# Kernel tuning notes

Hardware: AMD Instinct MI355X
Metric: run time of the kernel (lower is better)

Reference implementation:

```python
import jax, jax.numpy as jnp
import numpy as np

WALL_COT = 0.5   # init kwarg wall_cot
N_SEG = 64       # number of distinct segment ids (matches fill_max of segs)
MIN_FRAC = 0.01  # thresholds used in the torch loop


def _nearest_ds(x, He, We):
    """F.interpolate(x, size=(He,We), mode='nearest').squeeze(1) for x:[B,1,H,W].
    torch nearest picks src index floor(dst * H/He)."""
    B, _, H, W = x.shape
    iy = (jnp.arange(He) * H) // He
    ix = (jnp.arange(We) * W) // We
    return x[:, 0][:, iy][:, :, ix]  # [B,He,We]


def setup_inputs() -> dict:
    key = jax.random.key(0)
    ks = jax.random.split(key, 6)
    B, C_img, H, W = 8, 3, 512, 512
    C_feat, He, We = 64, 128, 128
    return {
        "outputs": jax.random.normal(ks[0], (B, C_img, H, W), dtype=jnp.float32),
        "inputs": jax.random.normal(ks[1], (B, C_img, H, W), dtype=jnp.float32),
        "enc1": jax.random.normal(ks[2], (B, C_feat, He, We), dtype=jnp.float32),
        "dec1": jax.random.normal(ks[3], (B, C_feat, He, We), dtype=jnp.float32),
        "masks": jax.random.uniform(ks[4], (B, 1, H, W), dtype=jnp.float32),
        "segs": jax.random.randint(ks[5], (B, 1, H, W), 0, N_SEG, dtype=jnp.int32),
        "confidence": jnp.zeros((1,), dtype=jnp.float32),
        "iteration": 1,
        "epoch": 0,
    }


def reference(outputs, inputs, enc1, dec1, masks, segs, confidence, iteration, epoch):
    B, _, He, We = enc1.shape
    npix = He * We

    # nearest-neighbor downsample of segment ids and cost masks to feature res
    seg_i = _nearest_ds(segs, He, We)            # [B,He,We] int
    mask_i = _nearest_ds(masks, He, We)          # [B,He,We]

    # per-pixel reconstruction error, mean over channels
    reco_error = jnp.mean((enc1 - dec1) ** 2, axis=1)  # [B,He,We]

    # segmented reductions: offset segment ids per batch item -> one flat pass
    flat_seg = (jnp.arange(B, dtype=jnp.int32)[:, None] * N_SEG
                + seg_i.reshape(B, -1)).reshape(-1)       # [B*He*We]
    f32 = reco_error.dtype
    counts = jax.ops.segment_sum(jnp.ones_like(flat_seg, dtype=f32), flat_seg,
                                 num_segments=B * N_SEG)  # [B*N_SEG]
    sum_err = jax.ops.segment_sum(reco_error.reshape(-1), flat_seg,
                                  num_segments=B * N_SEG)
    pos_px = ((mask_i > 0) & (mask_i < WALL_COT)).reshape(-1).astype(f32)
    pos_cnt = jax.ops.segment_sum(pos_px, flat_seg, num_segments=B * N_SEG)

    safe_cnt = jnp.maximum(counts, 1.0)
    mean_err = sum_err / safe_cnt                  # mean reco error per segment
    valid = (counts / npix) >= MIN_FRAC            # torch: skip if count frac < 0.01
    pos_flag = (pos_cnt / safe_cnt) > MIN_FRAC     # torch: pos/counts > 0.01
    sel = (valid & pos_flag).astype(f32)
    # flat_reco_error_pos.mean()
    flat_pos_mean = jnp.sum(mean_err * sel) / jnp.maximum(jnp.sum(sel), 1.0)

    # recovery loss: zero-out targets where mask >= wall_cot, masked mean
    targets = jnp.where(masks >= WALL_COT, jnp.zeros_like(inputs), inputs)  # bcast [B,1,H,W]
    mse_recov = jnp.sum((outputs - targets) ** 2, axis=1, keepdims=True)    # [B,1,H,W]
    m = (masks > 0).astype(f32)
    loss_recov = jnp.sum(mse_recov * m) / jnp.maximum(jnp.sum(m), 1.0)

    return loss_recov + flat_pos_mean
```

## Files before the change

kernel.cpp:

```cpp
#include <hip/hip_runtime.h>

#define BATCH   8
#define CIMG    3
#define HFULL   512
#define WFULL   512
#define HWFULL  (HFULL * WFULL)
#define CFEAT   64
#define HE      128
#define WE      128
#define HWE     (HE * WE)
#define NSEG    64
#define NBSEG   (BATCH * NSEG)
#define WALL_COT 0.5f
#define MIN_FRAC 0.01f

#define NBLK    2048

#define WS_CNT   0
#define WS_SUM   NBSEG
#define WS_POS   (2 * NBSEG)
#define WS_BNUM  (3 * NBSEG)
#define WS_BDEN  (3 * NBSEG + NBLK)
#define WS_ZERO_FLOATS (3 * NBSEG)

__global__ __launch_bounds__(256, 2) void confloss_main_kernel(
    const float* __restrict__ outputs, const float* __restrict__ inputs,
    const float* __restrict__ enc1,    const float* __restrict__ dec1,
    const float* __restrict__ masks,   const int* __restrict__ segs,
    float* __restrict__ ws)
{
    const int tid = threadIdx.x;
    const int i   = blockIdx.x * 256 + tid;

    __shared__ float s_cnt[NSEG], s_sum[NSEG], s_pos[NSEG];
    __shared__ float s_rn[4], s_rd[4];
    if (tid < NSEG) { s_cnt[tid] = 0.f; s_sum[tid] = 0.f; s_pos[tid] = 0.f; }
    __syncthreads();

    const int g  = i & 32767;
    const int c  = i >> 15;
    const int ba = g >> 12;
    const int ra = (g & 4095) * 4;
    const size_t abase = ((size_t)ba * CFEAT + (size_t)c * 4) * HWE + ra;
    const float* ep = enc1 + abase;
    const float* dp = dec1 + abase;
    const int ya = ra >> 7, xa = ra & (WE - 1);
    const int fb = ba * HWFULL + (ya * 4) * WFULL + xa * 4;
    const bool duty = (c == (g & 15));

    const int bb = i >> 16;
    const int rb = (i & 65535) * 4;
    const float* ob = outputs + (size_t)bb * (CIMG * HWFULL) + rb;
    const float* ib = inputs  + (size_t)bb * (CIMG * HWFULL) + rb;

    const float4 e0 = *(const float4*)(ep);
    const float4 e1 = *(const float4*)(ep + HWE);
    const float4 e2 = *(const float4*)(ep + 2 * HWE);
    const float4 e3 = *(const float4*)(ep + 3 * HWE);
    const float4 d0 = *(const float4*)(dp);
    const float4 d1 = *(const float4*)(dp + HWE);
    const float4 d2 = *(const float4*)(dp + 2 * HWE);
    const float4 d3 = *(const float4*)(dp + 3 * HWE);
    const float4 mB = *(const float4*)(masks + (size_t)bb * HWFULL + rb);
    const float4 o0 = *(const float4*)(ob);
    const float4 o1 = *(const float4*)(ob + HWFULL);
    const float4 o2 = *(const float4*)(ob + 2 * HWFULL);
    const float4 i0 = *(const float4*)(ib);
    const float4 i1 = *(const float4*)(ib + HWFULL);
    const float4 i2 = *(const float4*)(ib + 2 * HWFULL);
    const int s0 = segs[fb], s1 = segs[fb + 4], s2 = segs[fb + 8], s3 = segs[fb + 12];
    float mk0 = 1.f, mk1 = 1.f, mk2 = 1.f, mk3 = 1.f;
    if (duty) {
        mk0 = masks[fb];     mk1 = masks[fb + 4];
        mk2 = masks[fb + 8]; mk3 = masks[fb + 12];
    }

    float num = 0.f, den = 0.f;
    {
        float tgt, dd, mse;
        mse = 0.f;
        tgt = (mB.x >= WALL_COT) ? 0.f : i0.x; dd = o0.x - tgt; mse += dd * dd;
        tgt = (mB.x >= WALL_COT) ? 0.f : i1.x; dd = o1.x - tgt; mse += dd * dd;
        tgt = (mB.x >= WALL_COT) ? 0.f : i2.x; dd = o2.x - tgt; mse += dd * dd;
        if (mB.x > 0.f) { num += mse; den += 1.f; }
        mse = 0.f;
        tgt = (mB.y >= WALL_COT) ? 0.f : i0.y; dd = o0.y - tgt; mse += dd * dd;
        tgt = (mB.y >= WALL_COT) ? 0.f : i1.y; dd = o1.y - tgt; mse += dd * dd;
        tgt = (mB.y >= WALL_COT) ? 0.f : i2.y; dd = o2.y - tgt; mse += dd * dd;
        if (mB.y > 0.f) { num += mse; den += 1.f; }
        mse = 0.f;
        tgt = (mB.z >= WALL_COT) ? 0.f : i0.z; dd = o0.z - tgt; mse += dd * dd;
        tgt = (mB.z >= WALL_COT) ? 0.f : i1.z; dd = o1.z - tgt; mse += dd * dd;
        tgt = (mB.z >= WALL_COT) ? 0.f : i2.z; dd = o2.z - tgt; mse += dd * dd;
        if (mB.z > 0.f) { num += mse; den += 1.f; }
        mse = 0.f;
        tgt = (mB.w >= WALL_COT) ? 0.f : i0.w; dd = o0.w - tgt; mse += dd * dd;
        tgt = (mB.w >= WALL_COT) ? 0.f : i1.w; dd = o1.w - tgt; mse += dd * dd;
        tgt = (mB.w >= WALL_COT) ? 0.f : i2.w; dd = o2.w - tgt; mse += dd * dd;
        if (mB.w > 0.f) { num += mse; den += 1.f; }
    }

    {
        float t0, t1, t2, t3;
        t0 = e0.x - d0.x; t1 = e1.x - d1.x; t2 = e2.x - d2.x; t3 = e3.x - d3.x;
        const float p0 = (t0*t0 + t1*t1 + t2*t2 + t3*t3) * (1.0f / (float)CFEAT);
        t0 = e0.y - d0.y; t1 = e1.y - d1.y; t2 = e2.y - d2.y; t3 = e3.y - d3.y;
        const float p1 = (t0*t0 + t1*t1 + t2*t2 + t3*t3) * (1.0f / (float)CFEAT);
        t0 = e0.z - d0.z; t1 = e1.z - d1.z; t2 = e2.z - d2.z; t3 = e3.z - d3.z;
        const float p2 = (t0*t0 + t1*t1 + t2*t2 + t3*t3) * (1.0f / (float)CFEAT);
        t0 = e0.w - d0.w; t1 = e1.w - d1.w; t2 = e2.w - d2.w; t3 = e3.w - d3.w;
        const float p3 = (t0*t0 + t1*t1 + t2*t2 + t3*t3) * (1.0f / (float)CFEAT);
        atomicAdd(&s_sum[s0], p0);
        atomicAdd(&s_sum[s1], p1);
        atomicAdd(&s_sum[s2], p2);
        atomicAdd(&s_sum[s3], p3);
        if (duty) {
            atomicAdd(&s_cnt[s0], 1.f); if (mk0 > 0.f && mk0 < WALL_COT) atomicAdd(&s_pos[s0], 1.f);
            atomicAdd(&s_cnt[s1], 1.f); if (mk1 > 0.f && mk1 < WALL_COT) atomicAdd(&s_pos[s1], 1.f);
            atomicAdd(&s_cnt[s2], 1.f); if (mk2 > 0.f && mk2 < WALL_COT) atomicAdd(&s_pos[s2], 1.f);
            atomicAdd(&s_cnt[s3], 1.f); if (mk3 > 0.f && mk3 < WALL_COT) atomicAdd(&s_pos[s3], 1.f);
        }
    }

#pragma unroll
    for (int off = 32; off >= 1; off >>= 1) {
        num += __shfl_down(num, off);
        den += __shfl_down(den, off);
    }
    if ((tid & 63) == 0) { s_rn[tid >> 6] = num; s_rd[tid >> 6] = den; }
    __syncthreads();

    if (tid == 0) {
        ws[WS_BNUM + blockIdx.x] = s_rn[0] + s_rn[1] + s_rn[2] + s_rn[3];
        ws[WS_BDEN + blockIdx.x] = s_rd[0] + s_rd[1] + s_rd[2] + s_rd[3];
    }
    if (tid < NSEG) {
        const int gb = ba * NSEG + tid;
        atomicAdd(&ws[WS_SUM + gb], s_sum[tid]);
        const float cv = s_cnt[tid];
        if (cv != 0.f) atomicAdd(&ws[WS_CNT + gb], cv);
        const float pv = s_pos[tid];
        if (pv != 0.f) atomicAdd(&ws[WS_POS + gb], pv);
    }
}

__global__ __launch_bounds__(512) void confloss_finalize_kernel(
    const float* __restrict__ ws, float* __restrict__ out)
{
    const int t = threadIdx.x;
    float rn = 0.f, rd = 0.f;
#pragma unroll
    for (int k = 0; k < NBLK / 512; ++k) {
        rn += ws[WS_BNUM + t + k * 512];
        rd += ws[WS_BDEN + t + k * 512];
    }
    const float cnt = ws[WS_CNT + t];
    const float sum = ws[WS_SUM + t];
    const float pos = ws[WS_POS + t];
    const float safe = fmaxf(cnt, 1.0f);
    const float mean = sum / safe;
    const bool valid = (cnt / (float)HWE) >= MIN_FRAC;
    const bool posf  = (pos / safe) > MIN_FRAC;
    float sel = (valid && posf) ? 1.0f : 0.0f;
    float val = mean * sel;

#pragma unroll
    for (int off = 32; off >= 1; off >>= 1) {
        val += __shfl_down(val, off);
        sel += __shfl_down(sel, off);
        rn  += __shfl_down(rn,  off);
        rd  += __shfl_down(rd,  off);
    }
    __shared__ float sv[8], ss[8], sn[8], sd[8];
    const int wid = t >> 6;
    if ((t & 63) == 0) { sv[wid] = val; ss[wid] = sel; sn[wid] = rn; sd[wid] = rd; }
    __syncthreads();
    if (t == 0) {
        float tv = 0.f, ts = 0.f, tn = 0.f, td = 0.f;
#pragma unroll
        for (int w = 0; w < 8; ++w) { tv += sv[w]; ts += ss[w]; tn += sn[w]; td += sd[w]; }
        const float flat_pos_mean = tv / fmaxf(ts, 1.0f);
        const float loss_recov = tn / fmaxf(td, 1.0f);
        out[0] = loss_recov + flat_pos_mean;
    }
}

extern "C" void kernel_launch(void* const* d_in, const int* in_sizes, int n_in,
                              void* d_out, int out_size, void* d_ws, size_t ws_size,
                              hipStream_t stream) {
    const float* outputs = (const float*)d_in[0];
    const float* inputs  = (const float*)d_in[1];
    const float* enc1    = (const float*)d_in[2];
    const float* dec1    = (const float*)d_in[3];
    const float* masks   = (const float*)d_in[4];
    const int*   segs    = (const int*)d_in[5];
    float* ws  = (float*)d_ws;
    float* out = (float*)d_out;

    hipMemsetAsync(ws, 0, WS_ZERO_FLOATS * sizeof(float), stream);

    confloss_main_kernel<<<NBLK, 256, 0, stream>>>(
        outputs, inputs, enc1, dec1, masks, segs, ws);
    confloss_finalize_kernel<<<1, 512, 0, stream>>>(ws, out);
}
```

Measured before the change: 36.68 us.

## Stream enc/dec tiles via global_load_lds, per-wave shared bins, replicated global bins

Enc1/dec1 feature loads now go straight into LDS through the async global_load_lds builtin, which frees VGPRs. The other loads are pinned with empty asm and a single vmcnt wait so they all stay in flight together. Per-segment error sums in shared memory are split per wave to cut LDS atomic contention. Global segment bins are replicated 8 ways by block index to spread the global atomic traffic, and finalize sums the replicas. This costs 32KB of extra LDS per block, which may lower occupancy, and it relies on a hand-placed waitcnt.

```diff
diff --git a/kernel.cpp b/kernel.cpp
--- a/kernel.cpp
+++ b/kernel.cpp
@@ -1,4 +1,5 @@
 #include <hip/hip_runtime.h>
+#include <stdint.h>
 
 #define BATCH   8
 #define CIMG    3
@@ -15,13 +16,17 @@
 #define MIN_FRAC 0.01f
 
 #define NBLK    2048
-
-#define WS_CNT   0
-#define WS_SUM   NBSEG
-#define WS_POS   (2 * NBSEG)
-#define WS_BNUM  (3 * NBSEG)
-#define WS_BDEN  (3 * NBSEG + NBLK)
-#define WS_ZERO_FLOATS (3 * NBSEG)
+#define NREP    8
+
+#define WS_BINS_FLOATS (NREP * 3 * NBSEG)
+#define WS_BNUM  WS_BINS_FLOATS
+#define WS_BDEN  (WS_BINS_FLOATS + NBLK)
+#define WS_ZERO_FLOATS WS_BINS_FLOATS
+
+#define KEEPF4(v) asm volatile("" :: "v"((v).x), "v"((v).y), "v"((v).z), "v"((v).w))
+
+typedef uint32_t u32g __attribute__((address_space(1)));
+typedef uint32_t u32l __attribute__((address_space(3)));
 
 __global__ __launch_bounds__(256, 2) void confloss_main_kernel(
     const float* __restrict__ outputs, const float* __restrict__ inputs,
@@ -30,11 +35,17 @@
     float* __restrict__ ws)
 {
     const int tid = threadIdx.x;
+    const int w   = tid >> 6;
+    const int l   = tid & 63;
     const int i   = blockIdx.x * 256 + tid;
 
-    __shared__ float s_cnt[NSEG], s_sum[NSEG], s_pos[NSEG];
+    __shared__ float sA[4][8][256];
+    __shared__ float s_sumW[4][NSEG];
+    __shared__ float s_cnt[NSEG], s_pos[NSEG];
     __shared__ float s_rn[4], s_rd[4];
-    if (tid < NSEG) { s_cnt[tid] = 0.f; s_sum[tid] = 0.f; s_pos[tid] = 0.f; }
+
+    s_sumW[w][l] = 0.f;
+    if (tid < NSEG) { s_cnt[tid] = 0.f; s_pos[tid] = 0.f; }
     __syncthreads();
 
     const int g  = i & 32767;
@@ -44,23 +55,28 @@
     const size_t abase = ((size_t)ba * CFEAT + (size_t)c * 4) * HWE + ra;
     const float* ep = enc1 + abase;
     const float* dp = dec1 + abase;
-    const int ya = ra >> 7, xa = ra & (WE - 1);
-    const int fb = ba * HWFULL + (ya * 4) * WFULL + xa * 4;
-    const bool duty = (c == (g & 15));
+
+#if __has_builtin(__builtin_amdgcn_global_load_lds)
+#pragma unroll
+    for (int k = 0; k < 4; ++k)
+        __builtin_amdgcn_global_load_lds((const u32g*)(ep + (size_t)k * HWE),
+                                         (u32l*)(&sA[w][k][0]), 16, 0, 0);
+#pragma unroll
+    for (int k = 0; k < 4; ++k)
+        __builtin_amdgcn_global_load_lds((const u32g*)(dp + (size_t)k * HWE),
+                                         (u32l*)(&sA[w][4 + k][0]), 16, 0, 0);
+#else
+#pragma unroll
+    for (int k = 0; k < 4; ++k) {
+        *(float4*)&sA[w][k][l * 4]     = *(const float4*)(ep + (size_t)k * HWE);
+        *(float4*)&sA[w][4 + k][l * 4] = *(const float4*)(dp + (size_t)k * HWE);
+    }
+#endif
 
     const int bb = i >> 16;
     const int rb = (i & 65535) * 4;
     const float* ob = outputs + (size_t)bb * (CIMG * HWFULL) + rb;
     const float* ib = inputs  + (size_t)bb * (CIMG * HWFULL) + rb;
-
-    const float4 e0 = *(const float4*)(ep);
-    const float4 e1 = *(const float4*)(ep + HWE);
-    const float4 e2 = *(const float4*)(ep + 2 * HWE);
-    const float4 e3 = *(const float4*)(ep + 3 * HWE);
-    const float4 d0 = *(const float4*)(dp);
-    const float4 d1 = *(const float4*)(dp + HWE);
-    const float4 d2 = *(const float4*)(dp + 2 * HWE);
-    const float4 d3 = *(const float4*)(dp + 3 * HWE);
     const float4 mB = *(const float4*)(masks + (size_t)bb * HWFULL + rb);
     const float4 o0 = *(const float4*)(ob);
     const float4 o1 = *(const float4*)(ob + HWFULL);
@@ -68,13 +84,22 @@
     const float4 i0 = *(const float4*)(ib);
     const float4 i1 = *(const float4*)(ib + HWFULL);
     const float4 i2 = *(const float4*)(ib + 2 * HWFULL);
+
+    const int ya = ra >> 7, xa = ra & (WE - 1);
+    const int fb = ba * HWFULL + (ya * 4) * WFULL + xa * 4;
     const int s0 = segs[fb], s1 = segs[fb + 4], s2 = segs[fb + 8], s3 = segs[fb + 12];
+    const bool duty = (c == (g & 15));
     float mk0 = 1.f, mk1 = 1.f, mk2 = 1.f, mk3 = 1.f;
     if (duty) {
         mk0 = masks[fb];     mk1 = masks[fb + 4];
         mk2 = masks[fb + 8]; mk3 = masks[fb + 12];
     }
 
+    KEEPF4(mB); KEEPF4(o0); KEEPF4(o1); KEEPF4(o2);
+    KEEPF4(i0); KEEPF4(i1); KEEPF4(i2);
+    asm volatile("" :: "v"(s0), "v"(s1), "v"(s2), "v"(s3));
+    asm volatile("s_waitcnt vmcnt(0)" ::: "memory");
+
     float num = 0.f, den = 0.f;
     {
         float tgt, dd, mse;
@@ -101,19 +126,29 @@
     }
 
     {
+        const float4 E0 = *(const float4*)&sA[w][0][l * 4];
+        const float4 E1 = *(const float4*)&sA[w][1][l * 4];
+        const float4 E2 = *(const float4*)&sA[w][2][l * 4];
+        const float4 E3 = *(const float4*)&sA[w][3][l * 4];
+        const float4 D0 = *(const float4*)&sA[w][4][l * 4];
+        const float4 D1 = *(const float4*)&sA[w][5][l * 4];
+        const float4 D2 = *(const float4*)&sA[w][6][l * 4];
+        const float4 D3 = *(const float4*)&sA[w][7][l * 4];
+
         float t0, t1, t2, t3;
-        t0 = e0.x - d0.x; t1 = e1.x - d1.x; t2 = e2.x - d2.x; t3 = e3.x - d3.x;
+        t0 = E0.x - D0.x; t1 = E1.x - D1.x; t2 = E2.x - D2.x; t3 = E3.x - D3.x;
         const float p0 = (t0*t0 + t1*t1 + t2*t2 + t3*t3) * (1.0f / (float)CFEAT);
-        t0 = e0.y - d0.y; t1 = e1.y - d1.y; t2 = e2.y - d2.y; t3 = e3.y - d3.y;
+        t0 = E0.y - D0.y; t1 = E1.y - D1.y; t2 = E2.y - D2.y; t3 = E3.y - D3.y;
         const float p1 = (t0*t0 + t1*t1 + t2*t2 + t3*t3) * (1.0f / (float)CFEAT);
-        t0 = e0.z - d0.z; t1 = e1.z - d1.z; t2 = e2.z - d2.z; t3 = e3.z - d3.z;
+        t0 = E0.z - D0.z; t1 = E1.z - D1.z; t2 = E2.z - D2.z; t3 = E3.z - D3.z;
         const float p2 = (t0*t0 + t1*t1 + t2*t2 + t3*t3) * (1.0f / (float)CFEAT);
-        t0 = e0.w - d0.w; t1 = e1.w - d1.w; t2 = e2.w - d2.w; t3 = e3.w - d3.w;
+        t0 = E0.w - D0.w; t1 = E1.w - D1.w; t2 = E2.w - D2.w; t3 = E3.w - D3.w;
         const float p3 = (t0*t0 + t1*t1 + t2*t2 + t3*t3) * (1.0f / (float)CFEAT);
-        atomicAdd(&s_sum[s0], p0);
-        atomicAdd(&s_sum[s1], p1);
-        atomicAdd(&s_sum[s2], p2);
-        atomicAdd(&s_sum[s3], p3);
+
+        atomicAdd(&s_sumW[w][s0], p0);
+        atomicAdd(&s_sumW[w][s1], p1);
+        atomicAdd(&s_sumW[w][s2], p2);
+        atomicAdd(&s_sumW[w][s3], p3);
         if (duty) {
             atomicAdd(&s_cnt[s0], 1.f); if (mk0 > 0.f && mk0 < WALL_COT) atomicAdd(&s_pos[s0], 1.f);
             atomicAdd(&s_cnt[s1], 1.f); if (mk1 > 0.f && mk1 < WALL_COT) atomicAdd(&s_pos[s1], 1.f);
@@ -127,7 +162,7 @@
         num += __shfl_down(num, off);
         den += __shfl_down(den, off);
     }
-    if ((tid & 63) == 0) { s_rn[tid >> 6] = num; s_rd[tid >> 6] = den; }
+    if (l == 0) { s_rn[w] = num; s_rd[w] = den; }
     __syncthreads();
 
     if (tid == 0) {
@@ -135,12 +170,15 @@
         ws[WS_BDEN + blockIdx.x] = s_rd[0] + s_rd[1] + s_rd[2] + s_rd[3];
     }
     if (tid < NSEG) {
+        const int rep  = blockIdx.x & (NREP - 1);
+        float* bins = ws + rep * (3 * NBSEG);
         const int gb = ba * NSEG + tid;
-        atomicAdd(&ws[WS_SUM + gb], s_sum[tid]);
+        const float sv = s_sumW[0][tid] + s_sumW[1][tid] + s_sumW[2][tid] + s_sumW[3][tid];
+        if (sv != 0.f) atomicAdd(&bins[NBSEG + gb], sv);
         const float cv = s_cnt[tid];
-        if (cv != 0.f) atomicAdd(&ws[WS_CNT + gb], cv);
+        if (cv != 0.f) atomicAdd(&bins[gb], cv);
         const float pv = s_pos[tid];
-        if (pv != 0.f) atomicAdd(&ws[WS_POS + gb], pv);
+        if (pv != 0.f) atomicAdd(&bins[2 * NBSEG + gb], pv);
     }
 }
 
@@ -154,9 +192,14 @@
         rn += ws[WS_BNUM + t + k * 512];
         rd += ws[WS_BDEN + t + k * 512];
     }
-    const float cnt = ws[WS_CNT + t];
-    const float sum = ws[WS_SUM + t];
-    const float pos = ws[WS_POS + t];
+    float cnt = 0.f, sum = 0.f, pos = 0.f;
+#pragma unroll
+    for (int rep = 0; rep < NREP; ++rep) {
+        const float* bins = ws + rep * (3 * NBSEG);
+        cnt += bins[t];
+        sum += bins[NBSEG + t];
+        pos += bins[2 * NBSEG + t];
+    }
     const float safe = fmaxf(cnt, 1.0f);
     const float mean = sum / safe;
     const bool valid = (cnt / (float)HWE) >= MIN_FRAC;
```

Result: slower. 37.95 us (+3.5%).

## Fuse finalize into main kernel via last-block counter with replicated global bins

Applied to the files above, without the earlier changes.

Merges the separate finalize kernel into the main kernel: each block bumps a global counter and the last block reads all partial results and computes the final loss. Blocks grow to 512 threads and the grid is halved. Shared-memory histograms are now kept per wave to reduce LDS atomic contention, and global bin atomics are spread over 8 replicas to reduce contention on the same addresses. This saves one kernel launch and its serialization gap, at the cost of a fence, a counter atomic and slightly more LDS use.

```diff
diff --git a/kernel.cpp b/kernel.cpp
--- a/kernel.cpp
+++ b/kernel.cpp
@@ -1,4 +1,5 @@
 #include <hip/hip_runtime.h>
+#include <stdint.h>
 
 #define BATCH   8
 #define CIMG    3
@@ -14,28 +15,41 @@
 #define WALL_COT 0.5f
 #define MIN_FRAC 0.01f
 
-#define NBLK    2048
-
-#define WS_CNT   0
-#define WS_SUM   NBSEG
-#define WS_POS   (2 * NBSEG)
-#define WS_BNUM  (3 * NBSEG)
-#define WS_BDEN  (3 * NBSEG + NBLK)
-#define WS_ZERO_FLOATS (3 * NBSEG)
-
-__global__ __launch_bounds__(256, 2) void confloss_main_kernel(
+#define NBLK    1024
+#define BLKT    512
+#define NWAVE   8
+#define NREP    8
+
+#define WS_BINS_FLOATS (NREP * 3 * NBSEG)
+#define WS_CTR   WS_BINS_FLOATS
+#define WS_BNUM  (WS_CTR + 4)
+#define WS_BDEN  (WS_BNUM + NBLK)
+#define WS_ZERO_FLOATS (WS_CTR + 1)
+
+__device__ __forceinline__ float agent_load(const float* p) {
+    return __hip_atomic_load(p, __ATOMIC_RELAXED, __HIP_MEMORY_SCOPE_AGENT);
+}
+__device__ __forceinline__ void agent_store(float* p, float v) {
+    __hip_atomic_store(p, v, __ATOMIC_RELAXED, __HIP_MEMORY_SCOPE_AGENT);
+}
+
+__global__ __launch_bounds__(BLKT) void confloss_fused_kernel(
     const float* __restrict__ outputs, const float* __restrict__ inputs,
     const float* __restrict__ enc1,    const float* __restrict__ dec1,
     const float* __restrict__ masks,   const int* __restrict__ segs,
-    float* __restrict__ ws)
+    float* __restrict__ ws, float* __restrict__ out)
 {
     const int tid = threadIdx.x;
-    const int i   = blockIdx.x * 256 + tid;
-
-    __shared__ float s_cnt[NSEG], s_sum[NSEG], s_pos[NSEG];
-    __shared__ float s_rn[4], s_rd[4];
-    if (tid < NSEG) { s_cnt[tid] = 0.f; s_sum[tid] = 0.f; s_pos[tid] = 0.f; }
-    __syncthreads();
+    const int w   = tid >> 6;
+    const int l   = tid & 63;
+    const int i   = blockIdx.x * BLKT + tid;
+
+    __shared__ float s_sumW[NWAVE][NSEG];
+    __shared__ float s_cntW[NWAVE][NSEG];
+    __shared__ float s_posW[NWAVE][NSEG];
+    __shared__ float s_rn[NWAVE], s_rd[NWAVE];
+    __shared__ int   s_last;
+    s_sumW[w][l] = 0.f; s_cntW[w][l] = 0.f; s_posW[w][l] = 0.f;
 
     const int g  = i & 32767;
     const int c  = i >> 15;
@@ -44,9 +58,6 @@
     const size_t abase = ((size_t)ba * CFEAT + (size_t)c * 4) * HWE + ra;
     const float* ep = enc1 + abase;
     const float* dp = dec1 + abase;
-    const int ya = ra >> 7, xa = ra & (WE - 1);
-    const int fb = ba * HWFULL + (ya * 4) * WFULL + xa * 4;
-    const bool duty = (c == (g & 15));
 
     const int bb = i >> 16;
     const int rb = (i & 65535) * 4;
@@ -68,7 +79,11 @@
     const float4 i0 = *(const float4*)(ib);
     const float4 i1 = *(const float4*)(ib + HWFULL);
     const float4 i2 = *(const float4*)(ib + 2 * HWFULL);
+
+    const int ya = ra >> 7, xa = ra & (WE - 1);
+    const int fb = ba * HWFULL + (ya * 4) * WFULL + xa * 4;
     const int s0 = segs[fb], s1 = segs[fb + 4], s2 = segs[fb + 8], s3 = segs[fb + 12];
+    const bool duty = (c == (g & 15));
     float mk0 = 1.f, mk1 = 1.f, mk2 = 1.f, mk3 = 1.f;
     if (duty) {
         mk0 = masks[fb];     mk1 = masks[fb + 4];
@@ -110,15 +125,16 @@
         const float p2 = (t0*t0 + t1*t1 + t2*t2 + t3*t3) * (1.0f / (float)CFEAT);
         t0 = e0.w - d0.w; t1 = e1.w - d1.w; t2 = e2.w - d2.w; t3 = e3.w - d3.w;
         const float p3 = (t0*t0 + t1*t1 + t2*t2 + t3*t3) * (1.0f / (float)CFEAT);
-        atomicAdd(&s_sum[s0], p0);
-        atomicAdd(&s_sum[s1], p1);
-        atomicAdd(&s_sum[s2], p2);
-        atomicAdd(&s_sum[s3], p3);
+
+        atomicAdd(&s_sumW[w][s0], p0);
+        atomicAdd(&s_sumW[w][s1], p1);
+        atomicAdd(&s_sumW[w][s2], p2);
+        atomicAdd(&s_sumW[w][s3], p3);
         if (duty) {
-            atomicAdd(&s_cnt[s0], 1.f); if (mk0 > 0.f && mk0 < WALL_COT) atomicAdd(&s_pos[s0], 1.f);
-            atomicAdd(&s_cnt[s1], 1.f); if (mk1 > 0.f && mk1 < WALL_COT) atomicAdd(&s_pos[s1], 1.f);
-            atomicAdd(&s_cnt[s2], 1.f); if (mk2 > 0.f && mk2 < WALL_COT) atomicAdd(&s_pos[s2], 1.f);
-            atomicAdd(&s_cnt[s3], 1.f); if (mk3 > 0.f && mk3 < WALL_COT) atomicAdd(&s_pos[s3], 1.f);
+            atomicAdd(&s_cntW[w][s0], 1.f); if (mk0 > 0.f && mk0 < WALL_COT) atomicAdd(&s_posW[w][s0], 1.f);
+            atomicAdd(&s_cntW[w][s1], 1.f); if (mk1 > 0.f && mk1 < WALL_COT) atomicAdd(&s_posW[w][s1], 1.f);
+            atomicAdd(&s_cntW[w][s2], 1.f); if (mk2 > 0.f && mk2 < WALL_COT) atomicAdd(&s_posW[w][s2], 1.f);
+            atomicAdd(&s_cntW[w][s3], 1.f); if (mk3 > 0.f && mk3 < WALL_COT) atomicAdd(&s_posW[w][s3], 1.f);
         }
     }
 
@@ -127,61 +143,81 @@
         num += __shfl_down(num, off);
         den += __shfl_down(den, off);
     }
-    if ((tid & 63) == 0) { s_rn[tid >> 6] = num; s_rd[tid >> 6] = den; }
+    if (l == 0) { s_rn[w] = num; s_rd[w] = den; }
+
     __syncthreads();
 
+    if (tid < NSEG) {
+        float sv = 0.f, cv = 0.f, pv = 0.f;
+#pragma unroll
+        for (int k = 0; k < NWAVE; ++k) {
+            sv += s_sumW[k][tid]; cv += s_cntW[k][tid]; pv += s_posW[k][tid];
+        }
+        const int rep = blockIdx.x & (NREP - 1);
+        float* bins = ws + rep * (3 * NBSEG);
+        const int gb = ba * NSEG + tid;
+        if (cv != 0.f) atomicAdd(&bins[gb], cv);
+        if (sv != 0.f) atomicAdd(&bins[NBSEG + gb], sv);
+        if (pv != 0.f) atomicAdd(&bins[2 * NBSEG + gb], pv);
+    }
     if (tid == 0) {
-        ws[WS_BNUM + blockIdx.x] = s_rn[0] + s_rn[1] + s_rn[2] + s_rn[3];
-        ws[WS_BDEN + blockIdx.x] = s_rd[0] + s_rd[1] + s_rd[2] + s_rd[3];
-    }
-    if (tid < NSEG) {
-        const int gb = ba * NSEG + tid;
-        atomicAdd(&ws[WS_SUM + gb], s_sum[tid]);
-        const float cv = s_cnt[tid];
-        if (cv != 0.f) atomicAdd(&ws[WS_CNT + gb], cv);
-        const float pv = s_pos[tid];
-        if (pv != 0.f) atomicAdd(&ws[WS_POS + gb], pv);
-    }
-}
-
-__global__ __launch_bounds__(512) void confloss_finalize_kernel(
-    const float* __restrict__ ws, float* __restrict__ out)
-{
-    const int t = threadIdx.x;
-    float rn = 0.f, rd = 0.f;
-#pragma unroll
-    for (int k = 0; k < NBLK / 512; ++k) {
-        rn += ws[WS_BNUM + t + k * 512];
-        rd += ws[WS_BDEN + t + k * 512];
-    }
-    const float cnt = ws[WS_CNT + t];
-    const float sum = ws[WS_SUM + t];
-    const float pos = ws[WS_POS + t];
-    const float safe = fmaxf(cnt, 1.0f);
-    const float mean = sum / safe;
-    const bool valid = (cnt / (float)HWE) >= MIN_FRAC;
-    const bool posf  = (pos / safe) > MIN_FRAC;
-    float sel = (valid && posf) ? 1.0f : 0.0f;
-    float val = mean * sel;
-
-#pragma unroll
-    for (int off = 32; off >= 1; off >>= 1) {
-        val += __shfl_down(val, off);
-        sel += __shfl_down(sel, off);
-        rn  += __shfl_down(rn,  off);
-        rd  += __shfl_down(rd,  off);
-    }
-    __shared__ float sv[8], ss[8], sn[8], sd[8];
-    const int wid = t >> 6;
-    if ((t & 63) == 0) { sv[wid] = val; ss[wid] = sel; sn[wid] = rn; sd[wid] = rd; }
+        float tn = 0.f, td = 0.f;
+#pragma unroll
+        for (int k = 0; k < NWAVE; ++k) { tn += s_rn[k]; td += s_rd[k]; }
+        agent_store(&ws[WS_BNUM + blockIdx.x], tn);
+        agent_store(&ws[WS_BDEN + blockIdx.x], td);
+    }
     __syncthreads();
-    if (t == 0) {
-        float tv = 0.f, ts = 0.f, tn = 0.f, td = 0.f;
-#pragma unroll
-        for (int w = 0; w < 8; ++w) { tv += sv[w]; ts += ss[w]; tn += sn[w]; td += sd[w]; }
-        const float flat_pos_mean = tv / fmaxf(ts, 1.0f);
-        const float loss_recov = tn / fmaxf(td, 1.0f);
-        out[0] = loss_recov + flat_pos_mean;
+
+    if (tid == 0) {
+        __threadfence();
+        unsigned* ctr = (unsigned*)(ws + WS_CTR);
+        const unsigned old = atomicAdd(ctr, 1u);
+        s_last = (old == NBLK - 1) ? 1 : 0;
+    }
+    __syncthreads();
+
+    if (s_last) {
+        const int t = tid;
+        float cnt = 0.f, sum = 0.f, pos = 0.f;
+#pragma unroll
+        for (int rep = 0; rep < NREP; ++rep) {
+            const float* bins = ws + rep * (3 * NBSEG);
+            cnt += agent_load(&bins[t]);
+            sum += agent_load(&bins[NBSEG + t]);
+            pos += agent_load(&bins[2 * NBSEG + t]);
+        }
+        float rn = 0.f, rd = 0.f;
+#pragma unroll
+        for (int k = 0; k < NBLK / BLKT; ++k) {
+            rn += agent_load(&ws[WS_BNUM + t + k * BLKT]);
+            rd += agent_load(&ws[WS_BDEN + t + k * BLKT]);
+        }
+        const float safe = fmaxf(cnt, 1.0f);
+        const float mean = sum / safe;
+        const bool valid = (cnt / (float)HWE) >= MIN_FRAC;
+        const bool posf  = (pos / safe) > MIN_FRAC;
+        float sel = (valid && posf) ? 1.0f : 0.0f;
+        float val = mean * sel;
+
+#pragma unroll
+        for (int off = 32; off >= 1; off >>= 1) {
+            val += __shfl_down(val, off);
+            sel += __shfl_down(sel, off);
+            rn  += __shfl_down(rn,  off);
+            rd  += __shfl_down(rd,  off);
+        }
+        __shared__ float fv[NWAVE], fs[NWAVE], fn[NWAVE], fd[NWAVE];
+        if (l == 0) { fv[w] = val; fs[w] = sel; fn[w] = rn; fd[w] = rd; }
+        __syncthreads();
+        if (tid == 0) {
+            float tv = 0.f, ts = 0.f, tn = 0.f, td = 0.f;
+#pragma unroll
+            for (int k = 0; k < NWAVE; ++k) { tv += fv[k]; ts += fs[k]; tn += fn[k]; td += fd[k]; }
+            const float flat_pos_mean = tv / fmaxf(ts, 1.0f);
+            const float loss_recov = tn / fmaxf(td, 1.0f);
+            out[0] = loss_recov + flat_pos_mean;
+        }
     }
 }
 
@@ -199,7 +235,6 @@
 
     hipMemsetAsync(ws, 0, WS_ZERO_FLOATS * sizeof(float), stream);
 
-    confloss_main_kernel<<<NBLK, 256, 0, stream>>>(
-        outputs, inputs, enc1, dec1, masks, segs, ws);
-    confloss_finalize_kernel<<<1, 512, 0, stream>>>(ws, out);
-}
+    confloss_fused_kernel<<<NBLK, BLKT, 0, stream>>>(
+        outputs, inputs, enc1, dec1, masks, segs, ws, out);
+}
```

Result: slower. 69.34 us (+89.0%).

## Split fused loss kernel into streaming pass and separate segment-binning kernel

Applied to the files above, without the earlier changes.

Replaces the single fused kernel with a streaming kernel whose even and odd blocks handle the per-pixel reconstruction error and the recovery loss respectively. The per-pixel errors go to workspace, and a new small binning kernel then does the per-segment histogram with per-wave shared bins. The aim is to drop the redundant shared-memory atomics (the old path did 16x more sum atomics spread over all channel slices) and the mixed load pattern. In exchange it adds an extra kernel launch and a workspace round-trip for the per-pixel errors.

```diff
diff --git a/kernel.cpp b/kernel.cpp
--- a/kernel.cpp
+++ b/kernel.cpp
@@ -1,4 +1,5 @@
 #include <hip/hip_runtime.h>
+#include <stdint.h>
 
 #define BATCH   8
 #define CIMG    3
@@ -14,132 +15,160 @@
 #define WALL_COT 0.5f
 #define MIN_FRAC 0.01f
 
-#define NBLK    2048
+#define NTILE_A 2048
+#define NTILE_B 2048
+#define NBLK_STREAM (NTILE_A + NTILE_B)
 
 #define WS_CNT   0
 #define WS_SUM   NBSEG
 #define WS_POS   (2 * NBSEG)
 #define WS_BNUM  (3 * NBSEG)
-#define WS_BDEN  (3 * NBSEG + NBLK)
+#define WS_BDEN  (WS_BNUM + NTILE_B)
+#define WS_ERR   (WS_BDEN + NTILE_B)
 #define WS_ZERO_FLOATS (3 * NBSEG)
 
-__global__ __launch_bounds__(256, 2) void confloss_main_kernel(
+typedef float vf4 __attribute__((ext_vector_type(4)));
+
+__global__ __launch_bounds__(256) void confloss_stream_kernel(
     const float* __restrict__ outputs, const float* __restrict__ inputs,
     const float* __restrict__ enc1,    const float* __restrict__ dec1,
-    const float* __restrict__ masks,   const int* __restrict__ segs,
+    const float* __restrict__ masks,   float* __restrict__ ws)
+{
+    const int tid = threadIdx.x;
+    const int idx = blockIdx.x >> 1;
+
+    if ((blockIdx.x & 1) == 0) {
+        __shared__ vf4 s_part[16][16];
+        const int grp = tid & 15;
+        const int cs  = tid >> 4;
+        const int G   = idx * 16 + grp;
+        const int ba  = G >> 12;
+        const int r   = (G & 4095) * 4;
+        const size_t base = ((size_t)ba * CFEAT + (size_t)cs * 4) * HWE + r;
+        const float* ep = enc1 + base;
+        const float* dp = dec1 + base;
+
+        const vf4 e0 = *(const vf4*)(ep);
+        const vf4 e1 = *(const vf4*)(ep + HWE);
+        const vf4 e2 = *(const vf4*)(ep + 2 * HWE);
+        const vf4 e3 = *(const vf4*)(ep + 3 * HWE);
+        const vf4 d0 = *(const vf4*)(dp);
+        const vf4 d1 = *(const vf4*)(dp + HWE);
+        const vf4 d2 = *(const vf4*)(dp + 2 * HWE);
+        const vf4 d3 = *(const vf4*)(dp + 3 * HWE);
+
+        vf4 acc;
+        float t0, t1, t2, t3;
+        t0 = e0.x - d0.x; t1 = e1.x - d1.x; t2 = e2.x - d2.x; t3 = e3.x - d3.x;
+        acc.x = t0*t0 + t1*t1 + t2*t2 + t3*t3;
+        t0 = e0.y - d0.y; t1 = e1.y - d1.y; t2 = e2.y - d2.y; t3 = e3.y - d3.y;
+        acc.y = t0*t0 + t1*t1 + t2*t2 + t3*t3;
+        t0 = e0.z - d0.z; t1 = e1.z - d1.z; t2 = e2.z - d2.z; t3 = e3.z - d3.z;
+        acc.z = t0*t0 + t1*t1 + t2*t2 + t3*t3;
+        t0 = e0.w - d0.w; t1 = e1.w - d1.w; t2 = e2.w - d2.w; t3 = e3.w - d3.w;
+        acc.w = t0*t0 + t1*t1 + t2*t2 + t3*t3;
+
+        s_part[cs][grp] = acc;
+        __syncthreads();
+
+        if (tid < 16) {
+            vf4 s = s_part[0][tid];
+#pragma unroll
+            for (int k = 1; k < 16; ++k) {
+                const vf4 v = s_part[k][tid];
+                s.x += v.x; s.y += v.y; s.z += v.z; s.w += v.w;
+            }
+            const float sc = 1.0f / (float)CFEAT;
+            s.x *= sc; s.y *= sc; s.z *= sc; s.w *= sc;
+            *(vf4*)(ws + WS_ERR + (size_t)(idx * 16 + tid) * 4) = s;
+        }
+    } else {
+        const int g = idx * 256 + tid;
+        const int p = g * 4;
+        const int b = p >> 18;
+        const int r = p & (HWFULL - 1);
+        const float* ob = outputs + (size_t)b * (CIMG * HWFULL) + r;
+        const float* ib = inputs  + (size_t)b * (CIMG * HWFULL) + r;
+
+        const vf4 m4 = *(const vf4*)(masks + (size_t)b * HWFULL + r);
+        const vf4 o0 = *(const vf4*)(ob);
+        const vf4 o1 = *(const vf4*)(ob + HWFULL);
+        const vf4 o2 = *(const vf4*)(ob + 2 * HWFULL);
+        const vf4 i0 = *(const vf4*)(ib);
+        const vf4 i1 = *(const vf4*)(ib + HWFULL);
+        const vf4 i2 = *(const vf4*)(ib + 2 * HWFULL);
+
+        float num = 0.f, den = 0.f;
+#define BPIX(mv, a0, a1, a2, b0, b1, b2)                                    \
+        {                                                                   \
+            float tgt, dd, mse = 0.f;                                       \
+            tgt = ((mv) >= WALL_COT) ? 0.f : (b0); dd = (a0) - tgt; mse += dd*dd; \
+            tgt = ((mv) >= WALL_COT) ? 0.f : (b1); dd = (a1) - tgt; mse += dd*dd; \
+            tgt = ((mv) >= WALL_COT) ? 0.f : (b2); dd = (a2) - tgt; mse += dd*dd; \
+            if ((mv) > 0.f) { num += mse; den += 1.f; }                     \
+        }
+        BPIX(m4.x, o0.x, o1.x, o2.x, i0.x, i1.x, i2.x)
+        BPIX(m4.y, o0.y, o1.y, o2.y, i0.y, i1.y, i2.y)
+        BPIX(m4.z, o0.z, o1.z, o2.z, i0.z, i1.z, i2.z)
+        BPIX(m4.w, o0.w, o1.w, o2.w, i0.w, i1.w, i2.w)
+#undef BPIX
+
+#pragma unroll
+        for (int off = 32; off >= 1; off >>= 1) {
+            num += __shfl_down(num, off);
+            den += __shfl_down(den, off);
+        }
+        __shared__ float s_rn[4], s_rd[4];
+        const int w = tid >> 6;
+        if ((tid & 63) == 0) { s_rn[w] = num; s_rd[w] = den; }
+        __syncthreads();
+        if (tid == 0) {
+            ws[WS_BNUM + idx] = s_rn[0] + s_rn[1] + s_rn[2] + s_rn[3];
+            ws[WS_BDEN + idx] = s_rd[0] + s_rd[1] + s_rd[2] + s_rd[3];
+        }
+    }
+}
+
+__global__ __launch_bounds__(256) void confloss_bin_kernel(
+    const float* __restrict__ masks, const int* __restrict__ segs,
     float* __restrict__ ws)
 {
     const int tid = threadIdx.x;
-    const int i   = blockIdx.x * 256 + tid;
-
-    __shared__ float s_cnt[NSEG], s_sum[NSEG], s_pos[NSEG];
-    __shared__ float s_rn[4], s_rd[4];
-    if (tid < NSEG) { s_cnt[tid] = 0.f; s_sum[tid] = 0.f; s_pos[tid] = 0.f; }
+    const int w   = tid >> 6;
+    const int l   = tid & 63;
+    __shared__ float hc[4][NSEG], hs[4][NSEG], hp[4][NSEG];
+    hc[w][l] = 0.f; hs[w][l] = 0.f; hp[w][l] = 0.f;
+
+    const int gid = blockIdx.x * 256 + tid;
+    const int p   = gid * 4;
+    const int b   = p >> 14;
+    const int r   = p & (HWE - 1);
+    const int y   = r >> 7, x = r & (WE - 1);
+    const int src = b * HWFULL + (y * 4) * WFULL + x * 4;
+
+    const vf4 ev = *(const vf4*)(ws + WS_ERR + p);
+    const int   s0 = segs[src],      s1 = segs[src + 4],
+                s2 = segs[src + 8],  s3 = segs[src + 12];
+    const float m0 = masks[src],     m1 = masks[src + 4],
+                m2 = masks[src + 8], m3 = masks[src + 12];
+
+    atomicAdd(&hs[w][s0], ev.x); atomicAdd(&hc[w][s0], 1.f);
+    if (m0 > 0.f && m0 < WALL_COT) atomicAdd(&hp[w][s0], 1.f);
+    atomicAdd(&hs[w][s1], ev.y); atomicAdd(&hc[w][s1], 1.f);
+    if (m1 > 0.f && m1 < WALL_COT) atomicAdd(&hp[w][s1], 1.f);
+    atomicAdd(&hs[w][s2], ev.z); atomicAdd(&hc[w][s2], 1.f);
+    if (m2 > 0.f && m2 < WALL_COT) atomicAdd(&hp[w][s2], 1.f);
+    atomicAdd(&hs[w][s3], ev.w); atomicAdd(&hc[w][s3], 1.f);
+    if (m3 > 0.f && m3 < WALL_COT) atomicAdd(&hp[w][s3], 1.f);
     __syncthreads();
 
-    const int g  = i & 32767;
-    const int c  = i >> 15;
-    const int ba = g >> 12;
-    const int ra = (g & 4095) * 4;
-    const size_t abase = ((size_t)ba * CFEAT + (size_t)c * 4) * HWE + ra;
-    const float* ep = enc1 + abase;
-    const float* dp = dec1 + abase;
-    const int ya = ra >> 7, xa = ra & (WE - 1);
-    const int fb = ba * HWFULL + (ya * 4) * WFULL + xa * 4;
-    const bool duty = (c == (g & 15));
-
-    const int bb = i >> 16;
-    const int rb = (i & 65535) * 4;
-    const float* ob = outputs + (size_t)bb * (CIMG * HWFULL) + rb;
-    const float* ib = inputs  + (size_t)bb * (CIMG * HWFULL) + rb;
-
-    const float4 e0 = *(const float4*)(ep);
-    const float4 e1 = *(const float4*)(ep + HWE);
-    const float4 e2 = *(const float4*)(ep + 2 * HWE);
-    const float4 e3 = *(const float4*)(ep + 3 * HWE);
-    const float4 d0 = *(const float4*)(dp);
-    const float4 d1 = *(const float4*)(dp + HWE);
-    const float4 d2 = *(const float4*)(dp + 2 * HWE);
-    const float4 d3 = *(const float4*)(dp + 3 * HWE);
-    const float4 mB = *(const float4*)(masks + (size_t)bb * HWFULL + rb);
-    const float4 o0 = *(const float4*)(ob);
-    const float4 o1 = *(const float4*)(ob + HWFULL);
-    const float4 o2 = *(const float4*)(ob + 2 * HWFULL);
-    const float4 i0 = *(const float4*)(ib);
-    const float4 i1 = *(const float4*)(ib + HWFULL);
-    const float4 i2 = *(const float4*)(ib + 2 * HWFULL);
-    const int s0 = segs[fb], s1 = segs[fb + 4], s2 = segs[fb + 8], s3 = segs[fb + 12];
-    float mk0 = 1.f, mk1 = 1.f, mk2 = 1.f, mk3 = 1.f;
-    if (duty) {
-        mk0 = masks[fb];     mk1 = masks[fb + 4];
-        mk2 = masks[fb + 8]; mk3 = masks[fb + 12];
-    }
-
-    float num = 0.f, den = 0.f;
-    {
-        float tgt, dd, mse;
-        mse = 0.f;
-        tgt = (mB.x >= WALL_COT) ? 0.f : i0.x; dd = o0.x - tgt; mse += dd * dd;
-        tgt = (mB.x >= WALL_COT) ? 0.f : i1.x; dd = o1.x - tgt; mse += dd * dd;
-        tgt = (mB.x >= WALL_COT) ? 0.f : i2.x; dd = o2.x - tgt; mse += dd * dd;
-        if (mB.x > 0.f) { num += mse; den += 1.f; }
-        mse = 0.f;
-        tgt = (mB.y >= WALL_COT) ? 0.f : i0.y; dd = o0.y - tgt; mse += dd * dd;
-        tgt = (mB.y >= WALL_COT) ? 0.f : i1.y; dd = o1.y - tgt; mse += dd * dd;
-        tgt = (mB.y >= WALL_COT) ? 0.f : i2.y; dd = o2.y - tgt; mse += dd * dd;
-        if (mB.y > 0.f) { num += mse; den += 1.f; }
-        mse = 0.f;
-        tgt = (mB.z >= WALL_COT) ? 0.f : i0.z; dd = o0.z - tgt; mse += dd * dd;
-        tgt = (mB.z >= WALL_COT) ? 0.f : i1.z; dd = o1.z - tgt; mse += dd * dd;
-        tgt = (mB.z >= WALL_COT) ? 0.f : i2.z; dd = o2.z - tgt; mse += dd * dd;
-        if (mB.z > 0.f) { num += mse; den += 1.f; }
-        mse = 0.f;
-        tgt = (mB.w >= WALL_COT) ? 0.f : i0.w; dd = o0.w - tgt; mse += dd * dd;
-        tgt = (mB.w >= WALL_COT) ? 0.f : i1.w; dd = o1.w - tgt; mse += dd * dd;
-        tgt = (mB.w >= WALL_COT) ? 0.f : i2.w; dd = o2.w - tgt; mse += dd * dd;
-        if (mB.w > 0.f) { num += mse; den += 1.f; }
-    }
-
-    {
-        float t0, t1, t2, t3;
-        t0 = e0.x - d0.x; t1 = e1.x - d1.x; t2 = e2.x - d2.x; t3 = e3.x - d3.x;
-        const float p0 = (t0*t0 + t1*t1 + t2*t2 + t3*t3) * (1.0f / (float)CFEAT);
-        t0 = e0.y - d0.y; t1 = e1.y - d1.y; t2 = e2.y - d2.y; t3 = e3.y - d3.y;
-        const float p1 = (t0*t0 + t1*t1 + t2*t2 + t3*t3) * (1.0f / (float)CFEAT);
-        t0 = e0.z - d0.z; t1 = e1.z - d1.z; t2 = e2.z - d2.z; t3 = e3.z - d3.z;
-        const float p2 = (t0*t0 + t1*t1 + t2*t2 + t3*t3) * (1.0f / (float)CFEAT);
-        t0 = e0.w - d0.w; t1 = e1.w - d1.w; t2 = e2.w - d2.w; t3 = e3.w - d3.w;
-        const float p3 = (t0*t0 + t1*t1 + t2*t2 + t3*t3) * (1.0f / (float)CFEAT);
-        atomicAdd(&s_sum[s0], p0);
-        atomicAdd(&s_sum[s1], p1);
-        atomicAdd(&s_sum[s2], p2);
-        atomicAdd(&s_sum[s3], p3);
-        if (duty) {
-            atomicAdd(&s_cnt[s0], 1.f); if (mk0 > 0.f && mk0 < WALL_COT) atomicAdd(&s_pos[s0], 1.f);
-            atomicAdd(&s_cnt[s1], 1.f); if (mk1 > 0.f && mk1 < WALL_COT) atomicAdd(&s_pos[s1], 1.f);
-            atomicAdd(&s_cnt[s2], 1.f); if (mk2 > 0.f && mk2 < WALL_COT) atomicAdd(&s_pos[s2], 1.f);
-            atomicAdd(&s_cnt[s3], 1.f); if (mk3 > 0.f && mk3 < WALL_COT) atomicAdd(&s_pos[s3], 1.f);
-        }
-    }
-
-#pragma unroll
-    for (int off = 32; off >= 1; off >>= 1) {
-        num += __shfl_down(num, off);
-        den += __shfl_down(den, off);
-    }
-    if ((tid & 63) == 0) { s_rn[tid >> 6] = num; s_rd[tid >> 6] = den; }
-    __syncthreads();
-
-    if (tid == 0) {
-        ws[WS_BNUM + blockIdx.x] = s_rn[0] + s_rn[1] + s_rn[2] + s_rn[3];
-        ws[WS_BDEN + blockIdx.x] = s_rd[0] + s_rd[1] + s_rd[2] + s_rd[3];
-    }
     if (tid < NSEG) {
-        const int gb = ba * NSEG + tid;
-        atomicAdd(&ws[WS_SUM + gb], s_sum[tid]);
-        const float cv = s_cnt[tid];
+        const int gb = b * NSEG + tid;
+        const float cv = hc[0][tid] + hc[1][tid] + hc[2][tid] + hc[3][tid];
+        const float sv = hs[0][tid] + hs[1][tid] + hs[2][tid] + hs[3][tid];
+        const float pv = hp[0][tid] + hp[1][tid] + hp[2][tid] + hp[3][tid];
         if (cv != 0.f) atomicAdd(&ws[WS_CNT + gb], cv);
-        const float pv = s_pos[tid];
+        if (sv != 0.f) atomicAdd(&ws[WS_SUM + gb], sv);
         if (pv != 0.f) atomicAdd(&ws[WS_POS + gb], pv);
     }
 }
@@ -150,7 +179,7 @@
     const int t = threadIdx.x;
     float rn = 0.f, rd = 0.f;
 #pragma unroll
-    for (int k = 0; k < NBLK / 512; ++k) {
+    for (int k = 0; k < NTILE_B / 512; ++k) {
         rn += ws[WS_BNUM + t + k * 512];
         rd += ws[WS_BDEN + t + k * 512];
     }
@@ -178,7 +207,7 @@
     if (t == 0) {
         float tv = 0.f, ts = 0.f, tn = 0.f, td = 0.f;
 #pragma unroll
-        for (int w = 0; w < 8; ++w) { tv += sv[w]; ts += ss[w]; tn += sn[w]; td += sd[w]; }
+        for (int k = 0; k < 8; ++k) { tv += sv[k]; ts += ss[k]; tn += sn[k]; td += sd[k]; }
         const float flat_pos_mean = tv / fmaxf(ts, 1.0f);
         const float loss_recov = tn / fmaxf(td, 1.0f);
         out[0] = loss_recov + flat_pos_mean;
@@ -199,7 +228,8 @@
 
     hipMemsetAsync(ws, 0, WS_ZERO_FLOATS * sizeof(float), stream);
 
-    confloss_main_kernel<<<NBLK, 256, 0, stream>>>(
-        outputs, inputs, enc1, dec1, masks, segs, ws);
+    confloss_stream_kernel<<<NBLK_STREAM, 256, 0, stream>>>(
+        outputs, inputs, enc1, dec1, masks, ws);
+    confloss_bin_kernel<<<128, 256, 0, stream>>>(masks, segs, ws);
     confloss_finalize_kernel<<<1, 512, 0, stream>>>(ws, out);
 }
```

Measured after the change: 37.90 us. 1.03x slower.
